# Kernel tuning notes

Hardware: AMD Instinct MI355X
Metric: run time of the kernel (lower is better)

Reference implementation:

```python
import jax, jax.numpy as jnp
import numpy as np


def setup_inputs() -> dict:
    key = jax.random.key(0)
    qkv = jax.random.normal(key, (2, 1536, 4096), dtype=jnp.float32)
    return {"qkv": qkv, "num_heads": 8}


def reference(qkv, num_heads):
    bs, width, length = qkv.shape
    ch = width // (3 * num_heads)
    # [B*H, 3*ch, T] -> split into q, k, v each [B*H, ch, T]
    qkv_h = qkv.reshape(bs * num_heads, 3 * ch, length)
    q, k, v = qkv_h[:, :ch], qkv_h[:, ch:2 * ch], qkv_h[:, 2 * ch:]
    scale = 1.0 / np.sqrt(np.sqrt(ch)).astype(np.float32)
    # scores: [B*H, T, T]
    weight = jnp.einsum('bct,bcs->bts', q * scale, k * scale)
    weight = jax.nn.softmax(weight.astype(jnp.float32), axis=-1).astype(weight.dtype)
    a = jnp.einsum('bts,bcs->bct', weight, v)  # [B*H, ch, T]
    return a.reshape(bs, num_heads * ch, length)
```

## Files before the change

### kernel.cpp

```cpp
#include <hip/hip_runtime.h>
#include <hip/hip_bf16.h>

typedef __bf16 bf16x8 __attribute__((ext_vector_type(8)));
typedef float  f32x4  __attribute__((ext_vector_type(4)));

#define T_LEN 4096
#define QBLK  128
#define NT    64

__device__ __forceinline__ int swz(int row, int colByte) {
    return row * 128 + (colByte ^ (((row ^ (row >> 2)) & 7) << 4));
}
__device__ __forceinline__ int swzM(int row, int colByte) {
    return row * 128 + (colByte ^ ((row & 7) << 4));
}
__device__ __forceinline__ int swzO(int row, int colByte) {
    return row * 512 + (colByte ^ ((row & 7) << 5));
}

#define QSCALE 0.18033688011112042f

#if __has_builtin(__builtin_amdgcn_exp2f)
#define EXP2(x) __builtin_amdgcn_exp2f(x)
#else
__device__ __forceinline__ float EXP2(float x) {
    float r; asm("v_exp_f32 %0, %1" : "=v"(r) : "v"(x)); return r;
}
#endif

__global__ __launch_bounds__(256)
void qkv_prepass(const float* __restrict__ qkv, char* __restrict__ kpan,
                 char* __restrict__ vpan) {
    const int tile = blockIdx.x;
    const int bh   = blockIdx.y;
    const float* kp = qkv + ((size_t)bh * 192 + 64)  * T_LEN + tile * 64;
    const float* vp = qkv + ((size_t)bh * 192 + 128) * T_LEN + tile * 64;
    char* kout = kpan + (size_t)(bh * 64 + tile) * 8192;
    char* vout = vpan + (size_t)(bh * 64 + tile) * 8192;

    const int t = threadIdx.x;
    {
        const int s = t & 63;
        const int o4 = t >> 6;
        #pragma unroll
        for (int oo = 0; oo < 2; ++oo) {
            const int oct = o4 + oo * 4;
            bf16x8 v;
            #pragma unroll
            for (int j = 0; j < 8; ++j)
                v[j] = (__bf16)kp[(size_t)(oct * 8 + j) * T_LEN + s];
            const int chunk   = ((s >> 5) * 2 + (oct >> 2)) * 2 + ((s >> 4) & 1);
            const int lanepos = (oct & 3) * 16 + (s & 15);
            *(bf16x8*)(kout + chunk * 1024 + lanepos * 16) = v;
        }
    }
    {
        const int c = t & 63;
        #pragma unroll
        for (int lp = 0; lp < 2; ++lp) {
            const int hg = (t >> 6) + lp * 4;
            const int hf = hg >> 2, gg = hg & 3;
            float4 f0 = *(const float4*)(vp + (size_t)c * T_LEN + hf * 32 + gg * 4);
            float4 f1 = *(const float4*)(vp + (size_t)c * T_LEN + hf * 32 + 16 + gg * 4);
            bf16x8 v;
            v[0] = (__bf16)f0.x; v[1] = (__bf16)f0.y;
            v[2] = (__bf16)f0.z; v[3] = (__bf16)f0.w;
            v[4] = (__bf16)f1.x; v[5] = (__bf16)f1.y;
            v[6] = (__bf16)f1.z; v[7] = (__bf16)f1.w;
            const int chunk   = hf * 4 + (c >> 4);
            const int lanepos = gg * 16 + (c & 15);
            *(bf16x8*)(vout + chunk * 1024 + lanepos * 16) = v;
        }
    }
}

__global__ __launch_bounds__(512, 4)
void qkv_attn_l2(const float* __restrict__ qkv, float* __restrict__ out,
                 const char* __restrict__ kpan, const char* __restrict__ vpan) {
    __shared__ __align__(16) char lds[49152];

    const int fid   = (blockIdx.x & 7) * 64 + (blockIdx.x >> 3);
    const int bh    = fid >> 5;
    const int ttile = fid & 31;
    const float* qp = qkv + (size_t)bh * 192 * T_LEN;
    const int t0 = ttile * QBLK;

    const int tid  = threadIdx.x;
    const int wave = tid >> 6, lane = tid & 63;
    const int g = lane >> 4, i = lane & 15;
    const int tg = wave >> 1, half = wave & 1;

    const char* kbase = kpan + (size_t)bh * 64 * 8192 + half * 4096 + lane * 16;
    const char* vbase = vpan + (size_t)bh * 64 * 8192 + half * 4096 + lane * 16;

    {
        const int tq  = (tid & 31) * 4;
        const int cp8 = tid >> 5;
        #pragma unroll
        for (int hh = 0; hh < 2; ++hh) {
            const int cpair = cp8 + hh * 16;
            const float* base = qp + (size_t)(cpair * 2) * T_LEN + t0 + tq;
            float4 lo = *(const float4*)(base);
            float4 hi = *(const float4*)(base + T_LEN);
            __bf16 v0, v1;
            v0 = (__bf16)(lo.x * QSCALE); v1 = (__bf16)(hi.x * QSCALE);
            *(__bf16*)(lds + swz(tq + 0, cpair * 4)) = v0;
            *(__bf16*)(lds + swz(tq + 0, cpair * 4) + 2) = v1;
            v0 = (__bf16)(lo.y * QSCALE); v1 = (__bf16)(hi.y * QSCALE);
            *(__bf16*)(lds + swz(tq + 1, cpair * 4)) = v0;
            *(__bf16*)(lds + swz(tq + 1, cpair * 4) + 2) = v1;
            v0 = (__bf16)(lo.z * QSCALE); v1 = (__bf16)(hi.z * QSCALE);
            *(__bf16*)(lds + swz(tq + 2, cpair * 4)) = v0;
            *(__bf16*)(lds + swz(tq + 2, cpair * 4) + 2) = v1;
            v0 = (__bf16)(lo.w * QSCALE); v1 = (__bf16)(hi.w * QSCALE);
            *(__bf16*)(lds + swz(tq + 3, cpair * 4)) = v0;
            *(__bf16*)(lds + swz(tq + 3, cpair * 4) + 2) = v1;
        }
    }
    bf16x8 kf[4], vf[4];
    #pragma unroll
    for (int q = 0; q < 4; ++q) {
        kf[q] = *(const bf16x8*)(kbase + q * 1024);
        vf[q] = *(const bf16x8*)(vbase + q * 1024);
    }
    __syncthreads();
    bf16x8 qreg[2][2];
    #pragma unroll
    for (int h = 0; h < 2; ++h)
        #pragma unroll
        for (int kk = 0; kk < 2; ++kk)
            qreg[h][kk] = *(const bf16x8*)(lds + swz(tg * 32 + h * 16 + i, kk * 64 + g * 16));

    f32x4 oacc[2][4];
    #pragma unroll
    for (int h = 0; h < 2; ++h)
        #pragma unroll
        for (int n = 0; n < 4; ++n) oacc[h][n] = (f32x4){0.f, 0.f, 0.f, 0.f};
    float l0 = 0.f, l1 = 0.f;

    for (int t = 0; t < NT; ++t) {
        f32x4 sacc[2][2];
        #pragma unroll
        for (int h = 0; h < 2; ++h)
            #pragma unroll
            for (int mt = 0; mt < 2; ++mt) sacc[h][mt] = (f32x4){0.f, 0.f, 0.f, 0.f};
        __builtin_amdgcn_s_setprio(1);
        #pragma unroll
        for (int kk = 0; kk < 2; ++kk)
            #pragma unroll
            for (int mt = 0; mt < 2; ++mt) {
                sacc[0][mt] = __builtin_amdgcn_mfma_f32_16x16x32_bf16(kf[kk * 2 + mt], qreg[0][kk], sacc[0][mt], 0, 0, 0);
                sacc[1][mt] = __builtin_amdgcn_mfma_f32_16x16x32_bf16(kf[kk * 2 + mt], qreg[1][kk], sacc[1][mt], 0, 0, 0);
            }
        __builtin_amdgcn_s_setprio(0);
        if (t + 1 < NT) {
            const char* kn = kbase + (size_t)(t + 1) * 8192;
            #pragma unroll
            for (int q = 0; q < 4; ++q) kf[q] = *(const bf16x8*)(kn + q * 1024);
        }

        bf16x8 pa0, pa1;
        #pragma unroll
        for (int r = 0; r < 4; ++r) {
            float a0 = EXP2(sacc[0][0][r]);
            float a1 = EXP2(sacc[0][1][r]);
            l0 += a0 + a1;
            pa0[r] = (__bf16)a0; pa0[4 + r] = (__bf16)a1;
            float b0 = EXP2(sacc[1][0][r]);
            float b1 = EXP2(sacc[1][1][r]);
            l1 += b0 + b1;
            pa1[r] = (__bf16)b0; pa1[4 + r] = (__bf16)b1;
        }

        __builtin_amdgcn_s_setprio(1);
        #pragma unroll
        for (int n = 0; n < 4; ++n) {
            oacc[0][n] = __builtin_amdgcn_mfma_f32_16x16x32_bf16(pa0, vf[n], oacc[0][n], 0, 0, 0);
            oacc[1][n] = __builtin_amdgcn_mfma_f32_16x16x32_bf16(pa1, vf[n], oacc[1][n], 0, 0, 0);
        }
        __builtin_amdgcn_s_setprio(0);
        if (t + 1 < NT) {
            const char* vn = vbase + (size_t)(t + 1) * 8192;
            #pragma unroll
            for (int q = 0; q < 4; ++q) vf[q] = *(const bf16x8*)(vn + q * 1024);
        }
    }
    l0 += __shfl_xor(l0, 16); l0 += __shfl_xor(l0, 32);
    l1 += __shfl_xor(l1, 16); l1 += __shfl_xor(l1, 32);

    __syncthreads();
    char* mbase = lds + 16384 + tg * 8192;
    float* lbase = (float*)(lds);
    if (half == 1) {
        #pragma unroll
        for (int h = 0; h < 2; ++h)
            #pragma unroll
            for (int n = 0; n < 4; ++n)
                *(f32x4*)(mbase + swzM(n * 16 + i, h * 64 + g * 16)) = oacc[h][n];
        if (g == 0) { lbase[tg * 32 + i] = l0; lbase[tg * 32 + 16 + i] = l1; }
    }
    __syncthreads();
    if (half == 0) {
        #pragma unroll
        for (int h = 0; h < 2; ++h)
            #pragma unroll
            for (int n = 0; n < 4; ++n)
                oacc[h][n] += *(const f32x4*)(mbase + swzM(n * 16 + i, h * 64 + g * 16));
        l0 += lbase[tg * 32 + i];
        l1 += lbase[tg * 32 + 16 + i];
    }
    __syncthreads();
    if (half == 0) {
        #pragma unroll
        for (int h = 0; h < 2; ++h) {
            float invl = 1.0f / (h ? l1 : l0);
            #pragma unroll
            for (int reg = 0; reg < 4; ++reg) {
                float inv_r = __shfl(invl, g * 4 + reg);
                int t_loc = tg * 32 + h * 16 + g * 4 + reg;
                #pragma unroll
                for (int n = 0; n < 4; ++n) {
                    int c = n * 16 + i;
                    *(float*)(lds + swzO(c, t_loc * 4)) = oacc[h][n][reg] * inv_r;
                }
            }
        }
    }
    __syncthreads();
    #pragma unroll
    for (int it = 0; it < 4; ++it) {
        int idx = it * 512 + tid;
        int c   = idx >> 5;
        int seg = idx & 31;
        float4 u = *(const float4*)(lds + swzO(c, seg * 16));
        *(float4*)(out + (size_t)(bh * 64 + c) * T_LEN + t0 + seg * 4) = u;
    }
}

__global__ __launch_bounds__(256)
void simple_attn(const float* __restrict__ qkv, float* __restrict__ out) {
    const int wave = threadIdx.x >> 6;
    const int lane = threadIdx.x & 63;
    const int t  = blockIdx.x * 4 + wave;
    const int bh = blockIdx.y;
    const float* qp = qkv + (size_t)bh * 192 * T_LEN;
    const float* kp = qp + (size_t)64  * T_LEN;
    const float* vp = qp + (size_t)128 * T_LEN;
    const float qc = qp[(size_t)lane * T_LEN + t] * 0.125f;
    float m = -1e30f, l = 0.f, o = 0.f;
    for (int s = 0; s < T_LEN; ++s) {
        float prod = qc * kp[(size_t)lane * T_LEN + s];
        #pragma unroll
        for (int d = 1; d < 64; d <<= 1) prod += __shfl_xor(prod, d);
        const float nm   = fmaxf(m, prod);
        const float corr = __expf(m - nm);
        const float p    = __expf(prod - nm);
        l = l * corr + p;
        o = o * corr + p * vp[(size_t)lane * T_LEN + s];
        m = nm;
    }
    out[(size_t)(bh * 64 + lane) * T_LEN + t] = o / l;
}

extern "C" void kernel_launch(void* const* d_in, const int* in_sizes, int n_in,
                              void* d_out, int out_size, void* d_ws, size_t ws_size,
                              hipStream_t stream) {
    const float* qkv = (const float*)d_in[0];
    float* out = (float*)d_out;
    const size_t pan_bytes = (size_t)16 * 64 * 8192;
    if (ws_size >= 2 * pan_bytes) {
        char* kpan = (char*)d_ws;
        char* vpan = kpan + pan_bytes;
        qkv_prepass<<<dim3(64, 16), 256, 0, stream>>>(qkv, kpan, vpan);
        qkv_attn_l2<<<dim3(512), 512, 0, stream>>>(qkv, out, kpan, vpan);
    } else {
        simple_attn<<<dim3(T_LEN / 4, 16), 256, 0, stream>>>(qkv, out);
    }
}
```

Before: 95.36 us.

## Stage K tiles through double-buffered LDS with async global_load_lds, two tiles per iteration

The K panel is now written in the swizzled row layout and copied into double-buffered shared memory with global_load_lds. Each iteration prefetches the next pair of K tiles while it computes on the current pair, and all waves share the staged K instead of loading it per wave into registers. Each iteration also processes two 64-key tiles with V loaded directly into registers. The cost is a block-wide barrier every iteration, extra LDS reads for K fragments, and more register pressure from two sets of V fragments and score accumulators.

```diff
diff --git a/kernel.cpp b/kernel.cpp
--- a/kernel.cpp
+++ b/kernel.cpp
@@ -6,7 +6,7 @@
 
 #define T_LEN 4096
 #define QBLK  128
-#define NT    64
+#define NIT   32
 
 __device__ __forceinline__ int swz(int row, int colByte) {
     return row * 128 + (colByte ^ (((row ^ (row >> 2)) & 7) << 4));
@@ -27,6 +27,12 @@
     float r; asm("v_exp_f32 %0, %1" : "=v"(r) : "v"(x)); return r;
 }
 #endif
+
+__device__ __forceinline__ void glds16(const void* g, void* l) {
+    __builtin_amdgcn_global_load_lds(
+        (const __attribute__((address_space(1))) void*)g,
+        (__attribute__((address_space(3))) void*)l, 16, 0, 0);
+}
 
 __global__ __launch_bounds__(256)
 void qkv_prepass(const float* __restrict__ qkv, char* __restrict__ kpan,
@@ -40,7 +46,7 @@
 
     const int t = threadIdx.x;
     {
-        const int s = t & 63;
+        const int s  = t & 63;
         const int o4 = t >> 6;
         #pragma unroll
         for (int oo = 0; oo < 2; ++oo) {
@@ -49,9 +55,7 @@
             #pragma unroll
             for (int j = 0; j < 8; ++j)
                 v[j] = (__bf16)kp[(size_t)(oct * 8 + j) * T_LEN + s];
-            const int chunk   = ((s >> 5) * 2 + (oct >> 2)) * 2 + ((s >> 4) & 1);
-            const int lanepos = (oct & 3) * 16 + (s & 15);
-            *(bf16x8*)(kout + chunk * 1024 + lanepos * 16) = v;
+            *(bf16x8*)(kout + swz(s, oct * 16)) = v;
         }
     }
     {
@@ -75,14 +79,15 @@
 }
 
 __global__ __launch_bounds__(512, 4)
-void qkv_attn_l2(const float* __restrict__ qkv, float* __restrict__ out,
-                 const char* __restrict__ kpan, const char* __restrict__ vpan) {
+void qkv_attn_hyb(const float* __restrict__ qkv, float* __restrict__ out,
+                  const char* __restrict__ kpan, const char* __restrict__ vpan) {
     __shared__ __align__(16) char lds[49152];
 
     const int fid   = (blockIdx.x & 7) * 64 + (blockIdx.x >> 3);
     const int bh    = fid >> 5;
     const int ttile = fid & 31;
     const float* qp = qkv + (size_t)bh * 192 * T_LEN;
+    const char* kpb = kpan + (size_t)bh * 64 * 8192;
     const int t0 = ttile * QBLK;
 
     const int tid  = threadIdx.x;
@@ -90,8 +95,16 @@
     const int g = lane >> 4, i = lane & 15;
     const int tg = wave >> 1, half = wave & 1;
 
-    const char* kbase = kpan + (size_t)bh * 64 * 8192 + half * 4096 + lane * 16;
     const char* vbase = vpan + (size_t)bh * 64 * 8192 + half * 4096 + lane * 16;
+
+    glds16(kpb + tid * 16,        lds + 16384 + wave * 1024);
+    glds16(kpb + 8192 + tid * 16, lds + 16384 + 8192 + wave * 1024);
+    bf16x8 vf[2][4];
+    #pragma unroll
+    for (int q = 0; q < 4; ++q) {
+        vf[0][q] = *(const bf16x8*)(vbase + q * 1024);
+        vf[1][q] = *(const bf16x8*)(vbase + 8192 + q * 1024);
+    }
 
     {
         const int tq  = (tid & 31) * 4;
@@ -117,12 +130,6 @@
             *(__bf16*)(lds + swz(tq + 3, cpair * 4) + 2) = v1;
         }
     }
-    bf16x8 kf[4], vf[4];
-    #pragma unroll
-    for (int q = 0; q < 4; ++q) {
-        kf[q] = *(const bf16x8*)(kbase + q * 1024);
-        vf[q] = *(const bf16x8*)(vbase + q * 1024);
-    }
     __syncthreads();
     bf16x8 qreg[2][2];
     #pragma unroll
@@ -138,57 +145,72 @@
         for (int n = 0; n < 4; ++n) oacc[h][n] = (f32x4){0.f, 0.f, 0.f, 0.f};
     float l0 = 0.f, l1 = 0.f;
 
-    for (int t = 0; t < NT; ++t) {
-        f32x4 sacc[2][2];
-        #pragma unroll
-        for (int h = 0; h < 2; ++h)
-            #pragma unroll
-            for (int mt = 0; mt < 2; ++mt) sacc[h][mt] = (f32x4){0.f, 0.f, 0.f, 0.f};
+    for (int it = 0; it < NIT; ++it) {
+        if (it > 0) {
+            const char* vn = vbase + (size_t)(2 * it) * 8192;
+            #pragma unroll
+            for (int q = 0; q < 4; ++q) {
+                vf[0][q] = *(const bf16x8*)(vn + q * 1024);
+                vf[1][q] = *(const bf16x8*)(vn + 8192 + q * 1024);
+            }
+        }
+        if (it + 1 < NIT) {
+            const size_t off = (size_t)(2 * it + 2) * 8192;
+            const int b = (it + 1) & 1;
+            glds16(kpb + off + tid * 16,        lds + 16384 + b * 16384 + wave * 1024);
+            glds16(kpb + off + 8192 + tid * 16, lds + 16384 + b * 16384 + 8192 + wave * 1024);
+        }
+        char* KsB = lds + 16384 + (it & 1) * 16384;
+
+        f32x4 sacc[2][2][2];
+        #pragma unroll
+        for (int ta = 0; ta < 2; ++ta)
+            #pragma unroll
+            for (int h = 0; h < 2; ++h)
+                #pragma unroll
+                for (int mt = 0; mt < 2; ++mt) sacc[ta][h][mt] = (f32x4){0.f, 0.f, 0.f, 0.f};
         __builtin_amdgcn_s_setprio(1);
         #pragma unroll
-        for (int kk = 0; kk < 2; ++kk)
-            #pragma unroll
-            for (int mt = 0; mt < 2; ++mt) {
-                sacc[0][mt] = __builtin_amdgcn_mfma_f32_16x16x32_bf16(kf[kk * 2 + mt], qreg[0][kk], sacc[0][mt], 0, 0, 0);
-                sacc[1][mt] = __builtin_amdgcn_mfma_f32_16x16x32_bf16(kf[kk * 2 + mt], qreg[1][kk], sacc[1][mt], 0, 0, 0);
+        for (int ta = 0; ta < 2; ++ta)
+            #pragma unroll
+            for (int kk = 0; kk < 2; ++kk)
+                #pragma unroll
+                for (int mt = 0; mt < 2; ++mt) {
+                    bf16x8 kf = *(const bf16x8*)(KsB + ta * 8192 + swz(half * 32 + mt * 16 + i, kk * 64 + g * 16));
+                    sacc[ta][0][mt] = __builtin_amdgcn_mfma_f32_16x16x32_bf16(kf, qreg[0][kk], sacc[ta][0][mt], 0, 0, 0);
+                    sacc[ta][1][mt] = __builtin_amdgcn_mfma_f32_16x16x32_bf16(kf, qreg[1][kk], sacc[ta][1][mt], 0, 0, 0);
+                }
+        __builtin_amdgcn_s_setprio(0);
+
+        bf16x8 pa[2][2];
+        #pragma unroll
+        for (int ta = 0; ta < 2; ++ta)
+            #pragma unroll
+            for (int r = 0; r < 4; ++r) {
+                float a0 = EXP2(sacc[ta][0][0][r]);
+                float a1 = EXP2(sacc[ta][0][1][r]);
+                l0 += a0 + a1;
+                pa[ta][0][r] = (__bf16)a0; pa[ta][0][4 + r] = (__bf16)a1;
+                float b0 = EXP2(sacc[ta][1][0][r]);
+                float b1 = EXP2(sacc[ta][1][1][r]);
+                l1 += b0 + b1;
+                pa[ta][1][r] = (__bf16)b0; pa[ta][1][4 + r] = (__bf16)b1;
+            }
+
+        __builtin_amdgcn_s_setprio(1);
+        #pragma unroll
+        for (int ta = 0; ta < 2; ++ta)
+            #pragma unroll
+            for (int n = 0; n < 4; ++n) {
+                oacc[0][n] = __builtin_amdgcn_mfma_f32_16x16x32_bf16(pa[ta][0], vf[ta][n], oacc[0][n], 0, 0, 0);
+                oacc[1][n] = __builtin_amdgcn_mfma_f32_16x16x32_bf16(pa[ta][1], vf[ta][n], oacc[1][n], 0, 0, 0);
             }
         __builtin_amdgcn_s_setprio(0);
-        if (t + 1 < NT) {
-            const char* kn = kbase + (size_t)(t + 1) * 8192;
-            #pragma unroll
-            for (int q = 0; q < 4; ++q) kf[q] = *(const bf16x8*)(kn + q * 1024);
-        }
-
-        bf16x8 pa0, pa1;
-        #pragma unroll
-        for (int r = 0; r < 4; ++r) {
-            float a0 = EXP2(sacc[0][0][r]);
-            float a1 = EXP2(sacc[0][1][r]);
-            l0 += a0 + a1;
-            pa0[r] = (__bf16)a0; pa0[4 + r] = (__bf16)a1;
-            float b0 = EXP2(sacc[1][0][r]);
-            float b1 = EXP2(sacc[1][1][r]);
-            l1 += b0 + b1;
-            pa1[r] = (__bf16)b0; pa1[4 + r] = (__bf16)b1;
-        }
-
-        __builtin_amdgcn_s_setprio(1);
-        #pragma unroll
-        for (int n = 0; n < 4; ++n) {
-            oacc[0][n] = __builtin_amdgcn_mfma_f32_16x16x32_bf16(pa0, vf[n], oacc[0][n], 0, 0, 0);
-            oacc[1][n] = __builtin_amdgcn_mfma_f32_16x16x32_bf16(pa1, vf[n], oacc[1][n], 0, 0, 0);
-        }
-        __builtin_amdgcn_s_setprio(0);
-        if (t + 1 < NT) {
-            const char* vn = vbase + (size_t)(t + 1) * 8192;
-            #pragma unroll
-            for (int q = 0; q < 4; ++q) vf[q] = *(const bf16x8*)(vn + q * 1024);
-        }
+        __syncthreads();
     }
     l0 += __shfl_xor(l0, 16); l0 += __shfl_xor(l0, 32);
     l1 += __shfl_xor(l1, 16); l1 += __shfl_xor(l1, 32);
 
-    __syncthreads();
     char* mbase = lds + 16384 + tg * 8192;
     float* lbase = (float*)(lds);
     if (half == 1) {
@@ -272,7 +294,7 @@
         char* kpan = (char*)d_ws;
         char* vpan = kpan + pan_bytes;
         qkv_prepass<<<dim3(64, 16), 256, 0, stream>>>(qkv, kpan, vpan);
-        qkv_attn_l2<<<dim3(512), 512, 0, stream>>>(qkv, out, kpan, vpan);
+        qkv_attn_hyb<<<dim3(512), 512, 0, stream>>>(qkv, out, kpan, vpan);
     } else {
         simple_attn<<<dim3(T_LEN / 4, 16), 256, 0, stream>>>(qkv, out);
     }
```

Result: slower. 135.5 us (+42.1%).
